# Kernel tuning notes

Hardware: AMD Instinct MI355X
Metric: run time of the kernel (lower is better)

The kernel has to match this reference:

```python
import jax, jax.numpy as jnp
import numpy as np

N_NODES = 10000
N_EDGES = 320000
D = 256
L = 3
BN_EPS = 1e-5


def _segment_softmax(logits, seg, num_segments):
    # numerically stable softmax over variable-sized segments (incoming edges per node)
    m = jax.ops.segment_max(logits, seg, num_segments=num_segments)
    e = jnp.exp(logits - m[seg])
    s = jax.ops.segment_sum(e, seg, num_segments=num_segments)
    return e / s[seg]


def setup_inputs() -> dict:
    key = jax.random.key(0)
    ks = jax.random.split(key, 20)
    scale = 1.0 / np.sqrt(D)
    inp = {
        "x": jax.random.normal(ks[0], (N_NODES, D), dtype=jnp.float32),
        "edge_index": jax.random.randint(ks[1], (2, N_EDGES), 0, N_NODES, dtype=jnp.int64),
        # TransformerConv params (heads=1, concat=False)
        "Wq": jax.random.normal(ks[2], (D, D), jnp.float32) * scale,
        "bq": jnp.zeros((D,), jnp.float32),
        "Wk": jax.random.normal(ks[3], (D, D), jnp.float32) * scale,
        "bk": jnp.zeros((D,), jnp.float32),
        "Wv": jax.random.normal(ks[4], (D, D), jnp.float32) * scale,
        "bv": jnp.zeros((D,), jnp.float32),
        "Ws": jax.random.normal(ks[5], (D, D), jnp.float32) * scale,  # lin_skip (root weight)
        "bs": jnp.zeros((D,), jnp.float32),
        # SAGEConv params per layer: lin_l (neighbors, with bias), lin_r (root, no bias)
        "Wl": jax.random.normal(ks[6], (L, D, D), jnp.float32) * scale,
        "bl": jnp.zeros((L, D), jnp.float32),
        "Wr": jax.random.normal(ks[7], (L, D, D), jnp.float32) * scale,
        # BatchNorm affine params (eval mode: running_mean=0, running_var=1)
        "gamma": jnp.ones((L, D), jnp.float32) + 0.1 * jax.random.normal(ks[8], (L, D), jnp.float32),
        "beta": 0.1 * jax.random.normal(ks[9], (L, D), jnp.float32),
        # residual gate parameter (scalar)
        "alpha_res": jnp.asarray(0.5, jnp.float32),
    }
    return inp


def reference(x, edge_index, Wq, bq, Wk, bk, Wv, bv, Ws, bs, Wl, bl, Wr, gamma, beta, alpha_res):
    src, dst = edge_index[0], edge_index[1]  # message j -> i
    n, d = x.shape

    # ---- TransformerConv (heads=1, concat=False, eval: no dropout) ----
    q = x @ Wq + bq
    k = x @ Wk + bk
    v = x @ Wv + bv
    logits = jnp.sum(q[dst] * k[src], axis=-1) / jnp.sqrt(jnp.asarray(d, x.dtype))  # [E]
    attn = _segment_softmax(logits, dst, n)  # [E]
    agg = jax.ops.segment_sum(attn[:, None] * v[src], dst, num_segments=n)  # [N,D]
    h = agg + x @ Ws + bs  # root/skip connection
    h = jax.nn.relu(h)

    # in-degree for SAGE mean aggregation
    deg = jax.ops.segment_sum(jnp.ones((src.shape[0],), x.dtype), dst, num_segments=n)
    deg = jnp.maximum(deg, 1.0)[:, None]

    prev = h
    bn_scale = 1.0 / jnp.sqrt(1.0 + BN_EPS)  # eval-mode BN with running stats (0, 1)
    al = jax.nn.sigmoid(alpha_res)
    for i in range(Wl.shape[0]):
        mean_nb = jax.ops.segment_sum(h[src], dst, num_segments=n) / deg  # gather-mean-scatter
        z = mean_nb @ Wl[i] + bl[i] + h @ Wr[i]
        z = z * bn_scale * gamma[i] + beta[i]
        z = al * z + (1.0 - al) * prev
        h = jax.nn.relu(z)
        prev = h
    return h
```

## Files before the change

kernel.cpp:

```cpp
#include <hip/hip_runtime.h>
#include <hip/hip_bf16.h>

typedef unsigned short u16;
typedef unsigned int u32;
typedef __bf16 bf16x8 __attribute__((ext_vector_type(8)));
typedef float f32x4 __attribute__((ext_vector_type(4)));

#define DIM 256
#define BN_SCALE 0.9999950000374997f

__device__ __forceinline__ float bf2f(u16 u) {
    union { unsigned u; float f; } c; c.u = ((unsigned)u) << 16; return c.f;
}
__device__ __forceinline__ u16 f2bf(float f) {
    union { float f; unsigned u; } c; c.f = f;
    unsigned u = c.u;
    unsigned r = (u + 0x7FFFu + ((u >> 16) & 1u)) >> 16;
    return (u16)r;
}
__device__ __forceinline__ float asf(unsigned u) {
    union { unsigned u; float f; } c; c.u = u; return c.f;
}
__device__ __forceinline__ void cvt8(int4 v, float* f) {
    unsigned a0 = (unsigned)v.x, a1 = (unsigned)v.y, a2 = (unsigned)v.z, a3 = (unsigned)v.w;
    f[0] = asf(a0 << 16); f[1] = asf(a0 & 0xFFFF0000u);
    f[2] = asf(a1 << 16); f[3] = asf(a1 & 0xFFFF0000u);
    f[4] = asf(a2 << 16); f[5] = asf(a2 & 0xFFFF0000u);
    f[6] = asf(a3 << 16); f[7] = asf(a3 & 0xFFFF0000u);
}
__device__ __forceinline__ float dot8(const float* a, const float* b) {
    float s = a[0] * b[0];
    s += a[1] * b[1]; s += a[2] * b[2]; s += a[3] * b[3];
    s += a[4] * b[4]; s += a[5] * b[5]; s += a[6] * b[6]; s += a[7] * b[7];
    return s;
}
__device__ __forceinline__ void gl_lds16(const u16* g, u16* l) {
    __builtin_amdgcn_global_load_lds(
        (__attribute__((address_space(1))) const u32*)(const void*)g,
        (__attribute__((address_space(3))) u32*)(void*)l, 16, 0, 0);
}

__global__ void k_detect(const u16* __restrict__ xu, const long long* __restrict__ e64,
                         int* __restrict__ flags) {
    int lane = threadIdx.x;
    int plausible = 0;
#pragma unroll
    for (int j = 0; j < 4; ++j) {
        u16 u = xu[lane * 4 + j];
        int ex = (u >> 7) & 0xFF;
        plausible += (u == 0 || (ex >= 115 && ex <= 131)) ? 1 : 0;
    }
#pragma unroll
    for (int o = 32; o; o >>= 1) plausible += __shfl_xor(plausible, o, 64);
    long long hi = e64[lane] >> 32;
    unsigned long long b = __ballot(hi == 0);
    if (lane == 0) {
        flags[0] = (plausible >= 200) ? 1 : 0;
        flags[1] = (b == ~0ULL) ? 1 : 0;
    }
}

struct CvtDesc {
    const void* src[15];
    int cum[16];
};
__global__ void k_convert(CvtDesc d, const int* __restrict__ flags,
                          u16* __restrict__ arena, int total) {
    int i = blockIdx.x * 256 + threadIdx.x;
    if (i >= total) return;
    int t = 0;
    while (i >= d.cum[t + 1]) ++t;
    int j = i - d.cum[t];
    u16 v;
    if (flags[0]) v = ((const u16*)d.src[t])[j];
    else          v = f2bf(((const float*)d.src[t])[j]);
    arena[i] = v;
}

struct TDesc { const u16* src[12]; u16* dst[12]; };
__global__ __launch_bounds__(256) void k_transpose(TDesc td) {
    __shared__ u16 t[64][72];
    int m = blockIdx.x >> 4, tl = blockIdx.x & 15;
    int tr = (tl >> 2) * 64, tc = (tl & 3) * 64;
    const u16* S = td.src[m];
    u16* D = td.dst[m];
    int r = threadIdx.x >> 2, cs = (threadIdx.x & 3) * 16;
    *(int4*)&t[r][cs]     = *(const int4*)&S[(tr + r) * 256 + tc + cs];
    *(int4*)&t[r][cs + 8] = *(const int4*)&S[(tr + r) * 256 + tc + cs + 8];
    __syncthreads();
    u16 tmp[16];
#pragma unroll
    for (int j = 0; j < 16; ++j) tmp[j] = t[cs + j][r];
    *(int4*)&D[(tc + r) * 256 + tr + cs]     = *(int4*)&tmp[0];
    *(int4*)&D[(tc + r) * 256 + tr + cs + 8] = *(int4*)&tmp[8];
}

__global__ void k_edges(const int* __restrict__ ei32, const int* __restrict__ flags,
                        int* __restrict__ srcN, int* __restrict__ dstN,
                        int* __restrict__ deg, int E) {
    int e = blockIdx.x * 256 + threadIdx.x;
    if (e >= E) return;
    const long long* ei64 = (const long long*)ei32;
    int w64 = flags[1];
    int s = w64 ? (int)ei64[e]     : ei32[e];
    int d = w64 ? (int)ei64[E + e] : ei32[E + e];
    srcN[e] = s; dstN[e] = d;
    atomicAdd(&deg[d], 1);
}

__global__ __launch_bounds__(1024) void k_scan(const int* __restrict__ deg,
                                               int* __restrict__ offs,
                                               int* __restrict__ cursor, int N, int E) {
    __shared__ int s[1024];
    int t = threadIdx.x;
    int P = (N + 1023) >> 10;
    int base = t * P;
    int run = 0;
    for (int j = 0; j < P; ++j) { int idx = base + j; if (idx < N) run += deg[idx]; }
    s[t] = run;
    __syncthreads();
    int total = run;
    for (int off = 1; off < 1024; off <<= 1) {
        int v = 0;
        if (t >= off) v = s[t - off];
        __syncthreads();
        if (t >= off) s[t] += v;
        __syncthreads();
    }
    int r = s[t] - total;
    for (int j = 0; j < P; ++j) {
        int idx = base + j;
        if (idx < N) { offs[idx] = r; cursor[idx] = r; r += deg[idx]; }
    }
    if (t == 0) offs[N] = E;
}

__global__ void k_fill(const int* __restrict__ srcN, const int* __restrict__ dstN,
                       int* __restrict__ cursor, int* __restrict__ csr, int E) {
    int e = blockIdx.x * 256 + threadIdx.x;
    if (e < E) {
        int d = dstN[e];
        int pos = atomicAdd(&cursor[d], 1);
        csr[pos] = srcN[e];
    }
}

__global__ __launch_bounds__(256) void gemm_qkvs(
    const u16* __restrict__ x, const u16* __restrict__ WT,
    const u16* __restrict__ bias, u16* __restrict__ out, int M) {
    __shared__ __align__(16) u16 lds[16384];
    u16* As = lds;
    u16* Bs = lds + 8192;
    int tid = threadIdx.x, w = tid >> 6, lane = tid & 63;
    int l15 = lane & 15, quad = lane >> 4;
    int lr = lane >> 3, lc = lane & 7;
    int bm0 = blockIdx.x * 128, bn0 = blockIdx.y * 128;
    f32x4 acc[4][4];
#pragma unroll
    for (int a = 0; a < 4; ++a)
#pragma unroll
        for (int b = 0; b < 4; ++b) acc[a][b] = (f32x4){0.f, 0.f, 0.f, 0.f};

    for (int k0 = 0; k0 < 256; k0 += 64) {
#pragma unroll
        for (int j = 0; j < 4; ++j) {
            int ar = (w * 4 + j) * 8 + lr;
            int grow = bm0 + ar; if (grow >= M) grow = M - 1;
            gl_lds16(x + (size_t)grow * 256 + k0 + lc * 8, &As[(w * 4 + j) * 512]);
        }
#pragma unroll
        for (int j = 0; j < 4; ++j) {
            int nr = (w * 4 + j) * 8 + lr;
            gl_lds16(WT + (size_t)(bn0 + nr) * 256 + k0 + lc * 8, &Bs[(w * 4 + j) * 512]);
        }
        __syncthreads();
        int wm = w & 1, wn = w >> 1;
#pragma unroll
        for (int s = 0; s < 2; ++s) {
            bf16x8 a[4], b[4];
#pragma unroll
            for (int t = 0; t < 4; ++t)
                a[t] = *(const bf16x8*)&As[(wm * 64 + t * 16 + l15) * 64 + s * 32 + quad * 8];
#pragma unroll
            for (int t = 0; t < 4; ++t)
                b[t] = *(const bf16x8*)&Bs[(wn * 64 + t * 16 + l15) * 64 + s * 32 + quad * 8];
#pragma unroll
            for (int rt = 0; rt < 4; ++rt)
#pragma unroll
                for (int ct = 0; ct < 4; ++ct)
                    acc[rt][ct] = __builtin_amdgcn_mfma_f32_16x16x32_bf16(a[rt], b[ct], acc[rt][ct], 0, 0, 0);
        }
        __syncthreads();
    }
    int wm = w & 1, wn = w >> 1;
    u16* oL = lds + w * 4096;
#pragma unroll
    for (int rt = 0; rt < 4; ++rt)
#pragma unroll
        for (int ct = 0; ct < 4; ++ct) {
            int col = bn0 + wn * 64 + ct * 16 + l15;
            float bv = bf2f(bias[col]);
#pragma unroll
            for (int r = 0; r < 4; ++r)
                oL[(rt * 16 + quad * 4 + r) * 64 + ct * 16 + l15] = f2bf(acc[rt][ct][r] + bv);
        }
    __syncthreads();
#pragma unroll
    for (int j = 0; j < 8; ++j) {
        int orow = j * 8 + lr;
        int grow = bm0 + wm * 64 + orow;
        if (grow < M)
            *(int4*)&out[(size_t)grow * 1024 + bn0 + wn * 64 + lc * 8] = *(const int4*)&oL[orow * 64 + lc * 8];
    }
}

__global__ __launch_bounds__(256) void k_attn(const u16* __restrict__ qkvs,
                                              const int* __restrict__ csr,
                                              const int* __restrict__ offs,
                                              u16* __restrict__ hb, int N) {
    int wv = threadIdx.x >> 6, lane = threadIdx.x & 63;
    int i = blockIdx.x * 4 + wv;
    if (i >= N) return;
    size_t row = (size_t)i * 1024;
    int up = lane >> 5;
    int hl = lane & 31;
    float qf[8];
#pragma unroll
    for (int d = 0; d < 8; ++d) qf[d] = 0.f;
    if (!up) {
        int4 qv = *(const int4*)(qkvs + row + (unsigned)lane * 8);
        cvt8(qv, qf);
#pragma unroll
        for (int d = 0; d < 8; ++d) qf[d] *= 0.0625f;
    }
    int e0 = offs[i], e1 = offs[i + 1];
    float m = -1e30f, denom = 0.f;
    float acc[8];
#pragma unroll
    for (int d = 0; d < 8; ++d) acc[d] = 0.f;

    const u16* base = qkvs + 256 + (unsigned)lane * 8;
    int e = e0;
    for (; e + 4 <= e1; e += 4) {
        int s0 = csr[e], s1 = csr[e + 1], s2 = csr[e + 2], s3 = csr[e + 3];
        int4 r0 = *(const int4*)(base + (size_t)s0 * 1024);
        int4 r1 = *(const int4*)(base + (size_t)s1 * 1024);
        int4 r2 = *(const int4*)(base + (size_t)s2 * 1024);
        int4 r3 = *(const int4*)(base + (size_t)s3 * 1024);
        float f0[8], f1[8], f2[8], f3[8];
        cvt8(r0, f0); cvt8(r1, f1); cvt8(r2, f2); cvt8(r3, f3);
        float p0 = dot8(qf, f0), p1 = dot8(qf, f1), p2 = dot8(qf, f2), p3 = dot8(qf, f3);
#pragma unroll
        for (int o = 32; o; o >>= 1) {
            p0 += __shfl_xor(p0, o, 64);
            p1 += __shfl_xor(p1, o, 64);
            p2 += __shfl_xor(p2, o, 64);
            p3 += __shfl_xor(p3, o, 64);
        }
        float pm = fmaxf(fmaxf(p0, p1), fmaxf(p2, p3));
        if (pm > m) {
            float sc = __expf(m - pm);
            denom *= sc;
#pragma unroll
            for (int d = 0; d < 8; ++d) acc[d] *= sc;
            m = pm;
        }
        float w0 = __expf(p0 - m), w1 = __expf(p1 - m), w2 = __expf(p2 - m), w3 = __expf(p3 - m);
        denom += (w0 + w1) + (w2 + w3);
#pragma unroll
        for (int d = 0; d < 8; ++d)
            acc[d] += (w0 * f0[d] + w1 * f1[d]) + (w2 * f2[d] + w3 * f3[d]);
    }
    for (; e < e1; ++e) {
        int s0 = csr[e];
        int4 r0 = *(const int4*)(base + (size_t)s0 * 1024);
        float f0[8];
        cvt8(r0, f0);
        float p0 = dot8(qf, f0);
#pragma unroll
        for (int o = 32; o; o >>= 1) p0 += __shfl_xor(p0, o, 64);
        if (p0 > m) {
            float sc = __expf(m - p0);
            denom *= sc;
#pragma unroll
            for (int d = 0; d < 8; ++d) acc[d] *= sc;
            m = p0;
        }
        float w0 = __expf(p0 - m);
        denom += w0;
#pragma unroll
        for (int d = 0; d < 8; ++d) acc[d] += w0 * f0[d];
    }
    float inv = (denom > 0.f) ? 1.f / denom : 0.f;
    if (up) {
        int4 skv = *(const int4*)(qkvs + row + 768 + (unsigned)hl * 8);
        float sk[8];
        cvt8(skv, sk);
        u16 o16[8];
#pragma unroll
        for (int d = 0; d < 8; ++d) {
            float h = fmaxf(acc[d] * inv + sk[d], 0.f);
            o16[d] = f2bf(h);
        }
        *(int4*)(hb + (size_t)i * 256 + (unsigned)hl * 8) = *(const int4*)o16;
    }
}

__global__ __launch_bounds__(256) void k_agg(const u16* __restrict__ hin,
                                             const int* __restrict__ csr,
                                             const int* __restrict__ offs,
                                             u16* __restrict__ mean_out, int N) {
    int half = threadIdx.x >> 5, hl = threadIdx.x & 31;
    int i = blockIdx.x * 8 + half;
    if (i >= N) return;
    int e0 = offs[i], e1 = offs[i + 1];
    const u16* base = hin + (unsigned)hl * 8;
    float acc[8];
#pragma unroll
    for (int d = 0; d < 8; ++d) acc[d] = 0.f;
    int e = e0;
    for (; e + 4 <= e1; e += 4) {
        int s0 = csr[e], s1 = csr[e + 1], s2 = csr[e + 2], s3 = csr[e + 3];
        int4 r0 = *(const int4*)(base + (size_t)s0 * 256);
        int4 r1 = *(const int4*)(base + (size_t)s1 * 256);
        int4 r2 = *(const int4*)(base + (size_t)s2 * 256);
        int4 r3 = *(const int4*)(base + (size_t)s3 * 256);
        float f0[8], f1[8], f2[8], f3[8];
        cvt8(r0, f0); cvt8(r1, f1); cvt8(r2, f2); cvt8(r3, f3);
#pragma unroll
        for (int d = 0; d < 8; ++d) acc[d] += (f0[d] + f1[d]) + (f2[d] + f3[d]);
    }
    for (; e < e1; ++e) {
        int s0 = csr[e];
        int4 r0 = *(const int4*)(base + (size_t)s0 * 256);
        float f0[8];
        cvt8(r0, f0);
#pragma unroll
        for (int d = 0; d < 8; ++d) acc[d] += f0[d];
    }
    int dg = e1 - e0; if (dg < 1) dg = 1;
    float inv = 1.f / (float)dg;
    u16 o16[8];
#pragma unroll
    for (int d = 0; d < 8; ++d) o16[d] = f2bf(acc[d] * inv);
    *(int4*)(mean_out + (size_t)i * 256 + (unsigned)hl * 8) = *(const int4*)o16;
}

__global__ __launch_bounds__(256) void gemm_sage(
    const u16* __restrict__ meanA, const u16* __restrict__ hin,
    const u16* __restrict__ WlT, const u16* __restrict__ WrT,
    const u16* __restrict__ bl, const u16* __restrict__ gamma,
    const u16* __restrict__ beta, const u16* __restrict__ alpha,
    u16* __restrict__ hout, float* __restrict__ fout, int M) {
    __shared__ __align__(16) u16 lds[12288];
    u16* As = lds;
    u16* Bs = lds + 8192;
    int tid = threadIdx.x, w = tid >> 6, lane = tid & 63;
    int l15 = lane & 15, quad = lane >> 4;
    int lr = lane >> 3, lc = lane & 7;
    int bm0 = blockIdx.x * 128, n0 = blockIdx.y * 64;
    f32x4 acc[2][4];
#pragma unroll
    for (int a = 0; a < 2; ++a)
#pragma unroll
        for (int b = 0; b < 4; ++b) acc[a][b] = (f32x4){0.f, 0.f, 0.f, 0.f};

    for (int k0 = 0; k0 < 512; k0 += 64) {
        const u16* Asrc = (k0 < 256) ? meanA : hin;
        const u16* Bsrc = (k0 < 256) ? WlT : WrT;
        int kc = k0 & 255;
#pragma unroll
        for (int j = 0; j < 4; ++j) {
            int ar = (w * 4 + j) * 8 + lr;
            int grow = bm0 + ar; if (grow >= M) grow = M - 1;
            gl_lds16(Asrc + (size_t)grow * 256 + kc + lc * 8, &As[(w * 4 + j) * 512]);
        }
#pragma unroll
        for (int j = 0; j < 2; ++j) {
            int nr = (w * 2 + j) * 8 + lr;
            gl_lds16(Bsrc + (size_t)(n0 + nr) * 256 + kc + lc * 8, &Bs[(w * 2 + j) * 512]);
        }
        __syncthreads();
#pragma unroll
        for (int s = 0; s < 2; ++s) {
            bf16x8 a[2], b[4];
#pragma unroll
            for (int t = 0; t < 2; ++t)
                a[t] = *(const bf16x8*)&As[(w * 32 + t * 16 + l15) * 64 + s * 32 + quad * 8];
#pragma unroll
            for (int t = 0; t < 4; ++t)
                b[t] = *(const bf16x8*)&Bs[(t * 16 + l15) * 64 + s * 32 + quad * 8];
#pragma unroll
            for (int rt = 0; rt < 2; ++rt)
#pragma unroll
                for (int ct = 0; ct < 4; ++ct)
                    acc[rt][ct] = __builtin_amdgcn_mfma_f32_16x16x32_bf16(a[rt], b[ct], acc[rt][ct], 0, 0, 0);
        }
        __syncthreads();
    }

    float al = 1.f / (1.f + __expf(-bf2f(alpha[0])));
    float alc = 1.f - al;
    u16* oL = lds + w * 2048;
#pragma unroll
    for (int rt = 0; rt < 2; ++rt)
#pragma unroll
        for (int ct = 0; ct < 4; ++ct) {
            int col = n0 + ct * 16 + l15;
            float g  = bf2f(gamma[col]) * BN_SCALE;
            float be = bf2f(beta[col]);
            float bb = bf2f(bl[col]);
#pragma unroll
            for (int r = 0; r < 4; ++r) {
                int grow = bm0 + w * 32 + rt * 16 + quad * 4 + r;
                float z = (acc[rt][ct][r] + bb) * g + be;
                float prev = (grow < M) ? bf2f(hin[(size_t)grow * 256 + col]) : 0.f;
                z = al * z + alc * prev;
                z = fmaxf(z, 0.f);
                oL[(rt * 16 + quad * 4 + r) * 64 + ct * 16 + l15] = f2bf(z);
                if (fout && grow < M) fout[(size_t)grow * 256 + col] = z;
            }
        }
    __syncthreads();
#pragma unroll
    for (int j = 0; j < 4; ++j) {
        int orow = j * 8 + lr;
        int grow = bm0 + w * 32 + orow;
        if (grow < M)
            *(int4*)&hout[(size_t)grow * 256 + n0 + lc * 8] = *(const int4*)&oL[orow * 64 + lc * 8];
    }
}

extern "C" void kernel_launch(void* const* d_in, const int* in_sizes, int n_in,
                              void* d_out, int out_size, void* d_ws, size_t ws_size,
                              hipStream_t stream) {
    int N = in_sizes[0] / DIM;
    int E = in_sizes[1] / 2;
    int L = in_sizes[10] / (DIM * DIM);

    const int map[15] = {0, 2, 4, 6, 8, 10, 12, 3, 5, 7, 9, 11, 13, 14, 15};
    CvtDesc cd;
    cd.cum[0] = 0;
    for (int t = 0; t < 15; ++t) {
        cd.src[t] = d_in[map[t]];
        cd.cum[t + 1] = cd.cum[t] + in_sizes[map[t]];
    }
    int total = cd.cum[15];

    char* ws = (char*)d_ws;
    size_t off = 0;
    auto take = [&](size_t bytes) { size_t c = off; off = (off + bytes + 255) & ~255ULL; return c; };

    int* flags  = (int*)(ws + take(16));
    u16* arena  = (u16*)(ws + take((size_t)total * 2));
    u16* WT     = (u16*)(ws + take((size_t)(4 + 2 * L) * DIM * DIM * 2));
    int* srcN   = (int*)(ws + take((size_t)E * 4));
    int* dstN   = (int*)(ws + take((size_t)E * 4));
    int* csr    = (int*)(ws + take((size_t)E * 4));
    int* deg    = (int*)(ws + take((size_t)N * 4));
    int* offs   = (int*)(ws + take((size_t)(N + 1) * 4));
    int* cursor = (int*)(ws + take((size_t)N * 4));
    u16* hB0    = (u16*)(ws + take((size_t)N * DIM * 2));
    u16* qkvsB  = (u16*)(ws + take((size_t)N * 1024 * 2));
    u16* meanB  = qkvsB;
    u16* hB1    = qkvsB + (size_t)N * DIM;
    (void)ws_size; (void)n_in; (void)out_size;

    const u16* xb  = arena + cd.cum[0];
    const u16* Wqb = arena + cd.cum[1];
    const u16* Wkb = arena + cd.cum[2];
    const u16* Wvb = arena + cd.cum[3];
    const u16* Wsb = arena + cd.cum[4];
    const u16* Wlb = arena + cd.cum[5];
    const u16* Wrb = arena + cd.cum[6];
    const u16* biasF = arena + cd.cum[7];
    const u16* blb = arena + cd.cum[11];
    const u16* gmb = arena + cd.cum[12];
    const u16* btb = arena + cd.cum[13];
    const u16* alb = arena + cd.cum[14];

    k_detect<<<1, 64, 0, stream>>>((const u16*)d_in[0], (const long long*)d_in[1], flags);
    k_convert<<<(total + 255) / 256, 256, 0, stream>>>(cd, flags, arena, total);

    TDesc td;
    int nMat = 0;
    const u16* wsrc[4] = {Wqb, Wkb, Wvb, Wsb};
    for (int t = 0; t < 4; ++t) { td.src[nMat] = wsrc[t]; td.dst[nMat] = WT + (size_t)nMat * DIM * DIM; ++nMat; }
    for (int l = 0; l < L; ++l) { td.src[nMat] = Wlb + (size_t)l * DIM * DIM; td.dst[nMat] = WT + (size_t)nMat * DIM * DIM; ++nMat; }
    for (int l = 0; l < L; ++l) { td.src[nMat] = Wrb + (size_t)l * DIM * DIM; td.dst[nMat] = WT + (size_t)nMat * DIM * DIM; ++nMat; }
    k_transpose<<<nMat * 16, 256, 0, stream>>>(td);

    hipMemsetAsync(deg, 0, (size_t)N * 4, stream);
    int eb = (E + 255) / 256;
    k_edges<<<eb, 256, 0, stream>>>((const int*)d_in[1], flags, srcN, dstN, deg, E);
    k_scan<<<1, 1024, 0, stream>>>(deg, offs, cursor, N, E);
    k_fill<<<eb, 256, 0, stream>>>(srcN, dstN, cursor, csr, E);

    int Mb128 = (N + 127) / 128;
    gemm_qkvs<<<dim3(Mb128, 8), 256, 0, stream>>>(xb, WT, biasF, qkvsB, N);
    k_attn<<<(N + 3) / 4, 256, 0, stream>>>(qkvsB, csr, offs, hB0, N);

    for (int l = 0; l < L; ++l) {
        const u16* hin = (l & 1) ? hB1 : hB0;
        u16* hout      = (l & 1) ? hB0 : hB1;
        float* fout = (l == L - 1) ? (float*)d_out : nullptr;
        k_agg<<<(N + 7) / 8, 256, 0, stream>>>(hin, csr, offs, meanB, N);
        gemm_sage<<<dim3(Mb128, 4), 256, 0, stream>>>(
            meanB, hin, WT + (size_t)(4 + l) * DIM * DIM, WT + (size_t)(4 + L + l) * DIM * DIM,
            blb + (size_t)l * DIM, gmb + (size_t)l * DIM, btb + (size_t)l * DIM,
            alb, hout, fout, N);
    }
}
```

Measured before the change: 317.6 us.

## Process eight edges per wave in attention kernel and unroll aggregation to eight

The attention kernel is restructured so each wave handles eight edges at once, with eight lanes per edge each owning 32 dims. The old layout used a 64-lane dot product per edge where only half the lanes carried useful K or V work. The new one does short 8-lane reductions, a group-wide running max, and a final cross-group reduction of the accumulators. The SAGE aggregation kernel now issues eight gathers per iteration instead of four, exposing more memory-level parallelism. The cost is higher register pressure (32-float acc plus qf) and wasted lanes on nodes whose degree is not a multiple of eight.

```diff
diff --git a/kernel.cpp b/kernel.cpp
--- a/kernel.cpp
+++ b/kernel.cpp
@@ -221,88 +221,85 @@
     int wv = threadIdx.x >> 6, lane = threadIdx.x & 63;
     int i = blockIdx.x * 4 + wv;
     if (i >= N) return;
+    int sub = lane & 7;
+    int e8 = lane >> 3;
     size_t row = (size_t)i * 1024;
-    int up = lane >> 5;
-    int hl = lane & 31;
-    float qf[8];
-#pragma unroll
-    for (int d = 0; d < 8; ++d) qf[d] = 0.f;
-    if (!up) {
-        int4 qv = *(const int4*)(qkvs + row + (unsigned)lane * 8);
-        cvt8(qv, qf);
-#pragma unroll
-        for (int d = 0; d < 8; ++d) qf[d] *= 0.0625f;
+
+    float qf[32];
+    {
+        const u16* qp = qkvs + row + sub * 32;
+#pragma unroll
+        for (int j = 0; j < 4; ++j) {
+            int4 v = *(const int4*)(qp + j * 8);
+            float t[8]; cvt8(v, t);
+#pragma unroll
+            for (int d = 0; d < 8; ++d) qf[j * 8 + d] = t[d] * 0.0625f;
+        }
     }
     int e0 = offs[i], e1 = offs[i + 1];
     float m = -1e30f, denom = 0.f;
-    float acc[8];
-#pragma unroll
-    for (int d = 0; d < 8; ++d) acc[d] = 0.f;
-
-    const u16* base = qkvs + 256 + (unsigned)lane * 8;
-    int e = e0;
-    for (; e + 4 <= e1; e += 4) {
-        int s0 = csr[e], s1 = csr[e + 1], s2 = csr[e + 2], s3 = csr[e + 3];
-        int4 r0 = *(const int4*)(base + (size_t)s0 * 1024);
-        int4 r1 = *(const int4*)(base + (size_t)s1 * 1024);
-        int4 r2 = *(const int4*)(base + (size_t)s2 * 1024);
-        int4 r3 = *(const int4*)(base + (size_t)s3 * 1024);
-        float f0[8], f1[8], f2[8], f3[8];
-        cvt8(r0, f0); cvt8(r1, f1); cvt8(r2, f2); cvt8(r3, f3);
-        float p0 = dot8(qf, f0), p1 = dot8(qf, f1), p2 = dot8(qf, f2), p3 = dot8(qf, f3);
-#pragma unroll
-        for (int o = 32; o; o >>= 1) {
-            p0 += __shfl_xor(p0, o, 64);
-            p1 += __shfl_xor(p1, o, 64);
-            p2 += __shfl_xor(p2, o, 64);
-            p3 += __shfl_xor(p3, o, 64);
-        }
-        float pm = fmaxf(fmaxf(p0, p1), fmaxf(p2, p3));
+    float acc[32];
+#pragma unroll
+    for (int j = 0; j < 32; ++j) acc[j] = 0.f;
+
+    for (int base = e0; base < e1; base += 8) {
+        int e = base + e8;
+        int sidx = csr[(e < e1) ? e : (e1 - 1)];
+        const u16* kp = qkvs + (size_t)sidx * 1024 + 256 + sub * 32;
+        int4 kv[4], vv[4];
+#pragma unroll
+        for (int j = 0; j < 4; ++j) kv[j] = *(const int4*)(kp + j * 8);
+#pragma unroll
+        for (int j = 0; j < 4; ++j) vv[j] = *(const int4*)(kp + 256 + j * 8);
+        float p = 0.f;
+#pragma unroll
+        for (int j = 0; j < 4; ++j) { float t[8]; cvt8(kv[j], t); p += dot8(qf + j * 8, t); }
+        p += __shfl_xor(p, 1, 64);
+        p += __shfl_xor(p, 2, 64);
+        p += __shfl_xor(p, 4, 64);
+        if (e >= e1) p = -1e30f;
+        float pm = p;
+        pm = fmaxf(pm, __shfl_xor(pm, 8, 64));
+        pm = fmaxf(pm, __shfl_xor(pm, 16, 64));
+        pm = fmaxf(pm, __shfl_xor(pm, 32, 64));
         if (pm > m) {
             float sc = __expf(m - pm);
             denom *= sc;
 #pragma unroll
-            for (int d = 0; d < 8; ++d) acc[d] *= sc;
+            for (int j = 0; j < 32; ++j) acc[j] *= sc;
             m = pm;
         }
-        float w0 = __expf(p0 - m), w1 = __expf(p1 - m), w2 = __expf(p2 - m), w3 = __expf(p3 - m);
-        denom += (w0 + w1) + (w2 + w3);
-#pragma unroll
-        for (int d = 0; d < 8; ++d)
-            acc[d] += (w0 * f0[d] + w1 * f1[d]) + (w2 * f2[d] + w3 * f3[d]);
-    }
-    for (; e < e1; ++e) {
-        int s0 = csr[e];
-        int4 r0 = *(const int4*)(base + (size_t)s0 * 1024);
-        float f0[8];
-        cvt8(r0, f0);
-        float p0 = dot8(qf, f0);
-#pragma unroll
-        for (int o = 32; o; o >>= 1) p0 += __shfl_xor(p0, o, 64);
-        if (p0 > m) {
-            float sc = __expf(m - p0);
-            denom *= sc;
-#pragma unroll
-            for (int d = 0; d < 8; ++d) acc[d] *= sc;
-            m = p0;
-        }
-        float w0 = __expf(p0 - m);
-        denom += w0;
-#pragma unroll
-        for (int d = 0; d < 8; ++d) acc[d] += w0 * f0[d];
-    }
+        float w = __expf(p - m);
+        denom += w;
+#pragma unroll
+        for (int j = 0; j < 4; ++j) {
+            float t[8]; cvt8(vv[j], t);
+#pragma unroll
+            for (int d = 0; d < 8; ++d) acc[j * 8 + d] += w * t[d];
+        }
+    }
+    denom += __shfl_xor(denom, 8, 64);
+    denom += __shfl_xor(denom, 16, 64);
+    denom += __shfl_xor(denom, 32, 64);
     float inv = (denom > 0.f) ? 1.f / denom : 0.f;
-    if (up) {
-        int4 skv = *(const int4*)(qkvs + row + 768 + (unsigned)hl * 8);
-        float sk[8];
-        cvt8(skv, sk);
-        u16 o16[8];
-#pragma unroll
-        for (int d = 0; d < 8; ++d) {
-            float h = fmaxf(acc[d] * inv + sk[d], 0.f);
-            o16[d] = f2bf(h);
-        }
-        *(int4*)(hb + (size_t)i * 256 + (unsigned)hl * 8) = *(const int4*)o16;
+#pragma unroll
+    for (int j = 0; j < 32; ++j) {
+        acc[j] += __shfl_xor(acc[j], 8, 64);
+        acc[j] += __shfl_xor(acc[j], 16, 64);
+        acc[j] += __shfl_xor(acc[j], 32, 64);
+    }
+    if (e8 == 0) {
+        const u16* skp = qkvs + row + 768 + sub * 32;
+#pragma unroll
+        for (int j = 0; j < 4; ++j) {
+            int4 sv = *(const int4*)(skp + j * 8);
+            float t[8]; cvt8(sv, t);
+            u16 o[8];
+#pragma unroll
+            for (int d = 0; d < 8; ++d)
+                o[d] = f2bf(fmaxf(acc[j * 8 + d] * inv + t[d], 0.f));
+            *(int4*)(hb + (size_t)i * 256 + sub * 32 + j * 8) = *(const int4*)o;
+        }
     }
 }
 
@@ -319,24 +316,26 @@
 #pragma unroll
     for (int d = 0; d < 8; ++d) acc[d] = 0.f;
     int e = e0;
-    for (; e + 4 <= e1; e += 4) {
-        int s0 = csr[e], s1 = csr[e + 1], s2 = csr[e + 2], s3 = csr[e + 3];
-        int4 r0 = *(const int4*)(base + (size_t)s0 * 256);
-        int4 r1 = *(const int4*)(base + (size_t)s1 * 256);
-        int4 r2 = *(const int4*)(base + (size_t)s2 * 256);
-        int4 r3 = *(const int4*)(base + (size_t)s3 * 256);
-        float f0[8], f1[8], f2[8], f3[8];
-        cvt8(r0, f0); cvt8(r1, f1); cvt8(r2, f2); cvt8(r3, f3);
-#pragma unroll
-        for (int d = 0; d < 8; ++d) acc[d] += (f0[d] + f1[d]) + (f2[d] + f3[d]);
+    for (; e + 8 <= e1; e += 8) {
+        int4 r[8];
+#pragma unroll
+        for (int j = 0; j < 8; ++j) {
+            int s = csr[e + j];
+            r[j] = *(const int4*)(base + (size_t)s * 256);
+        }
+#pragma unroll
+        for (int j = 0; j < 8; ++j) {
+            float f[8]; cvt8(r[j], f);
+#pragma unroll
+            for (int d = 0; d < 8; ++d) acc[d] += f[d];
+        }
     }
     for (; e < e1; ++e) {
-        int s0 = csr[e];
-        int4 r0 = *(const int4*)(base + (size_t)s0 * 256);
-        float f0[8];
-        cvt8(r0, f0);
-#pragma unroll
-        for (int d = 0; d < 8; ++d) acc[d] += f0[d];
+        int s = csr[e];
+        int4 r0 = *(const int4*)(base + (size_t)s * 256);
+        float f[8]; cvt8(r0, f);
+#pragma unroll
+        for (int d = 0; d < 8; ++d) acc[d] += f[d];
     }
     int dg = e1 - e0; if (dg < 1) dg = 1;
     float inv = 1.f / (float)dg;
```

New measurement: 321.1 us. About the same (+1.1%).
